# Kernel tuning notes

Measured on AMD Instinct MI355X. Metric: run time of the kernel, lower is better.

The kernel has to match this reference:

```python
import jax, jax.numpy as jnp
import numpy as np

B, T, D, H = 4, 2048, 1024, 16
DH = D // H  # head dim = 64

def setup_inputs() -> dict:
    key = jax.random.key(0)
    k1, k2, k3, k4, k5, k6 = jax.random.split(key, 6)
    x = jax.random.normal(k1, (B, T, D), dtype=jnp.float32)
    mask = jax.random.randint(k2, (B, 1, 1, T), 0, 2, dtype=jnp.int32)
    # nn.Linear(out_dim, out_dim*3): weight stored here as [in, out]
    W_qkv = jax.random.normal(k3, (D, 3 * D), dtype=jnp.float32) * (1.0 / np.sqrt(D))
    b_qkv = jax.random.normal(k4, (3 * D,), dtype=jnp.float32) * 0.02
    W_out = jax.random.normal(k5, (D, D), dtype=jnp.float32) * (1.0 / np.sqrt(D))
    b_out = jax.random.normal(k6, (D,), dtype=jnp.float32) * 0.02
    return {"x": x, "mask": mask, "W_qkv": W_qkv, "b_qkv": b_qkv,
            "W_out": W_out, "b_out": b_out}

def reference(x, mask, W_qkv, b_qkv, W_out, b_out):
    # QKV projection: [B,T,3D]
    qkv = x @ W_qkv + b_qkv
    q, k, v = qkv[..., :D], qkv[..., D:2 * D], qkv[..., 2 * D:]
    # split heads -> [B,H,T,DH]
    def split(t):
        return t.reshape(B, T, H, DH).transpose(0, 2, 1, 3)
    q, k, v = split(q), split(k), split(v)
    # scaled dot-product attention (scale = sqrt(head_dim), per torch source)
    scores = jnp.einsum('bhqd,bhkd->bhqk', q, k) / jnp.sqrt(jnp.float32(DH))
    scores = jnp.where(mask == 0, jnp.float32(-1000.0), scores)
    weights = jax.nn.softmax(scores, axis=-1)  # dropout = identity (eval mode)
    out = jnp.einsum('bhqk,bhkd->bhqd', weights, v)
    out = out.transpose(0, 2, 1, 3).reshape(B, T, D)
    return out @ W_out + b_out
```

## Files before the change

### kernel.cpp

```cpp
#include <hip/hip_runtime.h>
#include <hip/hip_bf16.h>
#include <stdint.h>

#define B_  4
#define T_  2048
#define D_  1024
#define H_  16
#define DH_ 64

typedef _Float16 half8 __attribute__((ext_vector_type(8)));
typedef _Float16 half4 __attribute__((ext_vector_type(4)));
typedef float    f32x4 __attribute__((ext_vector_type(4)));

#define MFMA16(a, b, c) __builtin_amdgcn_mfma_f32_16x16x32_f16(a, b, c, 0, 0, 0)

__device__ static inline void gload_lds16(const void* g, void* l) {
  __builtin_amdgcn_global_load_lds(
      (const __attribute__((address_space(1))) void*)g,
      (__attribute__((address_space(3))) void*)l, 16, 0, 0);
}

__global__ void convert_f32_f16(const float* __restrict__ in, _Float16* __restrict__ out, long n) {
  long i = ((long)blockIdx.x * blockDim.x + threadIdx.x) * 4;
  long stride = (long)gridDim.x * blockDim.x * 4;
  for (; i < n; i += stride) {
    float4 v = *(const float4*)(in + i);
    half4 hv;
    hv.x = (_Float16)v.x; hv.y = (_Float16)v.y; hv.z = (_Float16)v.z; hv.w = (_Float16)v.w;
    *(half4*)(out + i) = hv;
  }
}

__global__ void make_maskh(const int* __restrict__ mask, _Float16* __restrict__ mh, int n) {
  int i = blockIdx.x * blockDim.x + threadIdx.x;
  if (i < n) mh[i] = mask[i] ? (_Float16)1.0f : (_Float16)0.0f;
}

__global__ void transpose_f32_f16(const float* __restrict__ in, _Float16* __restrict__ out,
                                  int K, int N) {
  __shared__ float tile[32][33];
  int n0 = blockIdx.x * 32, k0 = blockIdx.y * 32;
  int x = threadIdx.x, y = threadIdx.y;
  #pragma unroll
  for (int j = 0; j < 32; j += 8)
    tile[y + j][x] = in[(long)(k0 + y + j) * N + n0 + x];
  __syncthreads();
  #pragma unroll
  for (int j = 0; j < 32; j += 8)
    out[(long)(n0 + y + j) * K + k0 + x] = (_Float16)tile[x][y + j];
}

__global__ void vtrans_kernel(const _Float16* __restrict__ V, const _Float16* __restrict__ mh,
                              _Float16* __restrict__ Vt) {
  __shared__ _Float16 tl[64 * 73];
  const int t0 = blockIdx.x * 64;
  const int bh = blockIdx.y, b = bh >> 4;
  const long base = (long)bh * (T_ * DH_);
  const int t = threadIdx.x;
  #pragma unroll
  for (int i = 0; i < 2; ++i) {
    int c = t + i * 256;
    int row = c >> 3, cg = c & 7;
    _Float16 m = mh[b * T_ + t0 + row];
    half8 vv = *(const half8*)(V + base + (long)(t0 + row) * DH_ + cg * 8);
    #pragma unroll
    for (int j = 0; j < 8; ++j) vv[j] = vv[j] * m;
    *(half8*)&tl[row * 73 + cg * 8] = vv;
  }
  __syncthreads();
  #pragma unroll
  for (int i = 0; i < 2; ++i) {
    int c = t + i * 256;
    int dr = c >> 3, tg = c & 7;
    half8 v;
    #pragma unroll
    for (int j = 0; j < 8; ++j) v[j] = tl[(tg * 8 + j) * 73 + dr];
    *(half8*)(Vt + base + (long)dr * T_ + t0 + tg * 8) = v;
  }
}

template <int EPI>
__global__ __launch_bounds__(256, 2)
void mha_gemm(const _Float16* __restrict__ A, const _Float16* __restrict__ Bt,
              const float* __restrict__ bias,
              _Float16* __restrict__ qo, _Float16* __restrict__ ko, _Float16* __restrict__ vo,
              float* __restrict__ co, int M, int N, int K) {
  __shared__ _Float16 As[128 * 32];
  __shared__ _Float16 Bs[128 * 32];
  const int t = threadIdx.x;
  const int l = t & 63;
  const int w = t >> 6;
  const int wr = w >> 1, wc = w & 1;
  const int m0 = blockIdx.y * 128, n0 = blockIdx.x * 128;

  const _Float16* ag0 = A  + (long)(m0 +      w * 16 + (l >> 2)) * K + (l & 3) * 8;
  const _Float16* ag1 = A  + (long)(m0 + 64 + w * 16 + (l >> 2)) * K + (l & 3) * 8;
  const _Float16* bg0 = Bt + (long)(n0 +      w * 16 + (l >> 2)) * K + (l & 3) * 8;
  const _Float16* bg1 = Bt + (long)(n0 + 64 + w * 16 + (l >> 2)) * K + (l & 3) * 8;
  _Float16* la0 = &As[w * 512];
  _Float16* la1 = &As[2048 + w * 512];
  _Float16* lb0 = &Bs[w * 512];
  _Float16* lb1 = &Bs[2048 + w * 512];

  f32x4 acc[4][4];
  #pragma unroll
  for (int f = 0; f < 4; ++f)
    #pragma unroll
    for (int g = 0; g < 4; ++g) acc[f][g] = (f32x4){0.f, 0.f, 0.f, 0.f};

  const int ar = (wr * 64 + (l & 15)) * 32 + (l >> 4) * 8;
  const int br = (wc * 64 + (l & 15)) * 32 + (l >> 4) * 8;

  for (int k0 = 0; k0 < K; k0 += 32) {
    gload_lds16(ag0 + k0, la0);
    gload_lds16(ag1 + k0, la1);
    gload_lds16(bg0 + k0, lb0);
    gload_lds16(bg1 + k0, lb1);
    __syncthreads();
    half8 af[4], bf[4];
    #pragma unroll
    for (int f = 0; f < 4; ++f) af[f] = *(const half8*)&As[ar + f * 16 * 32];
    #pragma unroll
    for (int g = 0; g < 4; ++g) bf[g] = *(const half8*)&Bs[br + g * 16 * 32];
    #pragma unroll
    for (int f = 0; f < 4; ++f)
      #pragma unroll
      for (int g = 0; g < 4; ++g)
        acc[f][g] = MFMA16(af[f], bf[g], acc[f][g]);
    __syncthreads();
  }

  if constexpr (EPI == 0) {
    #pragma unroll
    for (int g = 0; g < 4; ++g) {
      int j = n0 + wc * 64 + g * 16 + (l & 15);
      float bv = bias[j];
      int which = j >> 10;
      int d = j & 1023;
      int h = d >> 6, dh = d & 63;
      _Float16* base = which == 0 ? qo : (which == 1 ? ko : vo);
      float sc = which == 0 ? 0.1803368801f : 1.0f;
      #pragma unroll
      for (int f = 0; f < 4; ++f) {
        int row0 = m0 + wr * 64 + f * 16 + ((l >> 4) << 2);
        #pragma unroll
        for (int r = 0; r < 4; ++r) {
          int row = row0 + r;
          int bb = row >> 11, tt = row & 2047;
          base[(((long)bb * H_ + h) * T_ + tt) * DH_ + dh] =
              (_Float16)((acc[f][g][r] + bv) * sc);
        }
      }
    }
  } else {
    #pragma unroll
    for (int g = 0; g < 4; ++g) {
      int j = n0 + wc * 64 + g * 16 + (l & 15);
      float bv = bias[j];
      #pragma unroll
      for (int f = 0; f < 4; ++f) {
        int row0 = m0 + wr * 64 + f * 16 + ((l >> 4) << 2);
        #pragma unroll
        for (int r = 0; r < 4; ++r)
          co[(long)(row0 + r) * N + j] = acc[f][g][r] + bv;
      }
    }
  }
}

__global__ __launch_bounds__(128, 2)
void mha_attn3(const _Float16* __restrict__ Q, const _Float16* __restrict__ K,
               const _Float16* __restrict__ Vt, const _Float16* __restrict__ mh,
               _Float16* __restrict__ out) {
  __shared__ _Float16 Ksh[2][4096];
  const int t = threadIdx.x, l = t & 63, w = t >> 6;
  const int hi = l >> 4, q = l & 15;

  const int bid = blockIdx.x;
  const int idx = bid >> 3;
  const int bh = (bid & 7) * 8 + (idx >> 4);
  const int qt = idx & 15;
  const int b = bh >> 4, h = bh & 15;
  const long base = (long)bh * (T_ * DH_);
  const int qb = qt * 128 + w * 64;

  half8 qf[4][2];
  #pragma unroll
  for (int G = 0; G < 4; ++G) {
    qf[G][0] = *(const half8*)(Q + base + (long)(qb + G * 16 + q) * DH_ + hi * 8);
    qf[G][1] = *(const half8*)(Q + base + (long)(qb + G * 16 + q) * DH_ + hi * 8 + 32);
  }

  const _Float16* ks[4];
  #pragma unroll
  for (int j = 0; j < 4; ++j) {
    int c = w * 256 + j * 64 + l;
    int row = c >> 3, sub = c & 7;
    int s = (sub ^ ((row & 7) ^ ((row >> 2) & 7))) * 8;
    ks[j] = K + base + row * DH_ + s;
  }

  int kcb[4];
  #pragma unroll
  for (int g = 0; g < 4; ++g) {
    int kr = (g >> 1) * 32 + (q >> 2) * 8 + (g & 1) * 4 + (q & 3);
    int sw = (kr & 7) ^ ((kr >> 2) & 7);
    kcb[g] = kr * 128 + ((hi * 16) ^ (sw << 4));
  }

  const _Float16* vsrc[4];
  #pragma unroll
  for (int o = 0; o < 4; ++o)
    vsrc[o] = Vt + base + (long)(o * 16 + q) * T_ + hi * 8;
  const _Float16* mrow = mh + b * T_ + hi * 8;

  f32x4 acc[4][4], accD[4];
  #pragma unroll
  for (int G = 0; G < 4; ++G) {
    accD[G] = (f32x4){0.f, 0.f, 0.f, 0.f};
    #pragma unroll
    for (int o = 0; o < 4; ++o) acc[G][o] = (f32x4){0.f, 0.f, 0.f, 0.f};
  }

  #pragma unroll
  for (int j = 0; j < 4; ++j)
    gload_lds16(ks[j], &Ksh[0][w * 2048 + j * 512]);
  __syncthreads();

  for (int kt = 0; kt < T_ / 64; ++kt) {
    const int bi = kt & 1;
    if (kt + 1 < T_ / 64) {
      #pragma unroll
      for (int j = 0; j < 4; ++j)
        gload_lds16(ks[j] + (kt + 1) * (64 * DH_), &Ksh[bi ^ 1][w * 2048 + j * 512]);
    }

    half8 vf[4][2];
    #pragma unroll
    for (int o = 0; o < 4; ++o) {
      vf[o][0] = *(const half8*)(vsrc[o] + kt * 64);
      vf[o][1] = *(const half8*)(vsrc[o] + kt * 64 + 32);
    }
    const half8 mf0 = *(const half8*)(mrow + kt * 64);
    const half8 mf1 = *(const half8*)(mrow + kt * 64 + 32);

    const char* kbb = (const char*)Ksh[bi];
    half8 kf[4][2];
    #pragma unroll
    for (int g = 0; g < 4; ++g) {
      kf[g][0] = *(const half8*)(kbb + kcb[g]);
      kf[g][1] = *(const half8*)(kbb + (kcb[g] ^ 64));
    }

    #pragma unroll
    for (int G = 0; G < 4; ++G) {
      f32x4 z[4];
      #pragma unroll
      for (int g = 0; g < 4; ++g) {
        f32x4 zz = (f32x4){0.f, 0.f, 0.f, 0.f};
        zz = MFMA16(kf[g][0], qf[G][0], zz);
        z[g] = MFMA16(kf[g][1], qf[G][1], zz);
      }
      half8 p0, p1;
      #pragma unroll
      for (int r = 0; r < 4; ++r) {
        p0[r]     = (_Float16)__builtin_amdgcn_exp2f(z[0][r]);
        p0[4 + r] = (_Float16)__builtin_amdgcn_exp2f(z[1][r]);
        p1[r]     = (_Float16)__builtin_amdgcn_exp2f(z[2][r]);
        p1[4 + r] = (_Float16)__builtin_amdgcn_exp2f(z[3][r]);
      }
      accD[G] = MFMA16(p0, mf0, accD[G]);
      accD[G] = MFMA16(p1, mf1, accD[G]);
      #pragma unroll
      for (int o = 0; o < 4; ++o) {
        acc[G][o] = MFMA16(p0, vf[o][0], acc[G][o]);
        acc[G][o] = MFMA16(p1, vf[o][1], acc[G][o]);
      }
    }
    __syncthreads();
  }

  #pragma unroll
  for (int G = 0; G < 4; ++G)
    #pragma unroll
    for (int r = 0; r < 4; ++r) {
      float inv = __builtin_amdgcn_rcpf(accD[G][r]);
      int trow = qb + G * 16 + hi * 4 + r;
      #pragma unroll
      for (int o = 0; o < 4; ++o)
        out[((long)b * T_ + trow) * D_ + h * DH_ + o * 16 + q] =
            (_Float16)(acc[G][o][r] * inv);
    }
}

extern "C" void kernel_launch(void* const* d_in, const int* in_sizes, int n_in,
                              void* d_out, int out_size, void* d_ws, size_t ws_size,
                              hipStream_t stream) {
  const float* x    = (const float*)d_in[0];
  const int*   mask = (const int*)d_in[1];
  const float* wqkv = (const float*)d_in[2];
  const float* bqkv = (const float*)d_in[3];
  const float* wout = (const float*)d_in[4];
  const float* bout = (const float*)d_in[5];
  float* out = (float*)d_out;

  _Float16* ws = (_Float16*)d_ws;
  const long nX = (long)B_ * T_ * D_;
  _Float16* xh    = ws;
  _Float16* wqkvt = xh + nX;
  _Float16* woutt = wqkvt + (long)D_ * 3 * D_;
  _Float16* mh    = woutt + (long)D_ * D_;
  _Float16* Qb    = woutt + (long)D_ * D_ + 16384;
  _Float16* Kb    = Qb + nX;
  _Float16* Vb    = Kb + nX;
  _Float16* attnh = Vb + nX;
  _Float16* Vtg   = xh;

  convert_f32_f16<<<2048, 256, 0, stream>>>(x, xh, nX);
  make_maskh<<<(B_ * T_) / 256, 256, 0, stream>>>(mask, mh, B_ * T_);
  transpose_f32_f16<<<dim3(3 * D_ / 32, D_ / 32), dim3(32, 8), 0, stream>>>(wqkv, wqkvt, D_, 3 * D_);
  transpose_f32_f16<<<dim3(D_ / 32, D_ / 32), dim3(32, 8), 0, stream>>>(wout, woutt, D_, D_);

  mha_gemm<0><<<dim3(3 * D_ / 128, B_ * T_ / 128), 256, 0, stream>>>(
      xh, wqkvt, bqkv, Qb, Kb, Vb, nullptr, B_ * T_, 3 * D_, D_);

  vtrans_kernel<<<dim3(T_ / 64, B_ * H_), 256, 0, stream>>>(Vb, mh, Vtg);

  mha_attn3<<<1024, 128, 0, stream>>>(Qb, Kb, Vtg, mh, attnh);

  mha_gemm<1><<<dim3(D_ / 128, B_ * T_ / 128), 256, 0, stream>>>(
      attnh, woutt, bout, nullptr, nullptr, nullptr, out, B_ * T_, D_, D_);
}
```

Before: 208.5 us.

## Deepen GEMM K-tile with swizzled LDS, remap blocks, halve attention query tile

The GEMM now loads 64-wide K tiles into XOR-swizzled LDS, which halves the number of barriers per K and avoids bank conflicts. It also maps a 1D grid so that consecutive blocks spread across XCDs, aiming for better L2 locality. The attention kernel processes 32 query rows per wave instead of 64, doubling the grid to 2048 blocks and lowering register pressure. It also raises wave priority around the MFMA section and packs the exp results with cvt_pkrtz. The cost is that each K/V tile is loaded twice as many times overall in attention, and the LDS footprint of the GEMM doubles.

```diff
diff --git a/kernel.cpp b/kernel.cpp
--- a/kernel.cpp
+++ b/kernel.cpp
@@ -10,6 +10,7 @@
 
 typedef _Float16 half8 __attribute__((ext_vector_type(8)));
 typedef _Float16 half4 __attribute__((ext_vector_type(4)));
+typedef __fp16   fp16x2 __attribute__((ext_vector_type(2)));
 typedef float    f32x4 __attribute__((ext_vector_type(4)));
 
 #define MFMA16(a, b, c) __builtin_amdgcn_mfma_f32_16x16x32_f16(a, b, c, 0, 0, 0)
@@ -81,26 +82,31 @@
 
 template <int EPI>
 __global__ __launch_bounds__(256, 2)
-void mha_gemm(const _Float16* __restrict__ A, const _Float16* __restrict__ Bt,
-              const float* __restrict__ bias,
-              _Float16* __restrict__ qo, _Float16* __restrict__ ko, _Float16* __restrict__ vo,
-              float* __restrict__ co, int M, int N, int K) {
-  __shared__ _Float16 As[128 * 32];
-  __shared__ _Float16 Bs[128 * 32];
+void mha_gemm2(const _Float16* __restrict__ A, const _Float16* __restrict__ Bt,
+               const float* __restrict__ bias,
+               _Float16* __restrict__ qo, _Float16* __restrict__ ko, _Float16* __restrict__ vo,
+               float* __restrict__ co, int M, int N, int K, int gx) {
+  __shared__ _Float16 As[128 * 64];
+  __shared__ _Float16 Bs[128 * 64];
   const int t = threadIdx.x;
   const int l = t & 63;
   const int w = t >> 6;
   const int wr = w >> 1, wc = w & 1;
-  const int m0 = blockIdx.y * 128, n0 = blockIdx.x * 128;
-
-  const _Float16* ag0 = A  + (long)(m0 +      w * 16 + (l >> 2)) * K + (l & 3) * 8;
-  const _Float16* ag1 = A  + (long)(m0 + 64 + w * 16 + (l >> 2)) * K + (l & 3) * 8;
-  const _Float16* bg0 = Bt + (long)(n0 +      w * 16 + (l >> 2)) * K + (l & 3) * 8;
-  const _Float16* bg1 = Bt + (long)(n0 + 64 + w * 16 + (l >> 2)) * K + (l & 3) * 8;
-  _Float16* la0 = &As[w * 512];
-  _Float16* la1 = &As[2048 + w * 512];
-  _Float16* lb0 = &Bs[w * 512];
-  _Float16* lb1 = &Bs[2048 + w * 512];
+
+  const int cpx = gridDim.x >> 3;
+  const int wg = (blockIdx.x & 7) * cpx + (blockIdx.x >> 3);
+  const int m0 = (wg / gx) * 128, n0 = (wg % gx) * 128;
+
+  const _Float16* ag[4];
+  const _Float16* bg[4];
+  #pragma unroll
+  for (int j = 0; j < 4; ++j) {
+    int c = j * 256 + t;
+    int row = c >> 3, sub = c & 7;
+    int s = (sub ^ (row & 7)) * 8;
+    ag[j] = A  + (long)(m0 + row) * K + s;
+    bg[j] = Bt + (long)(n0 + row) * K + s;
+  }
 
   f32x4 acc[4][4];
   #pragma unroll
@@ -108,25 +114,34 @@
     #pragma unroll
     for (int g = 0; g < 4; ++g) acc[f][g] = (f32x4){0.f, 0.f, 0.f, 0.f};
 
-  const int ar = (wr * 64 + (l & 15)) * 32 + (l >> 4) * 8;
-  const int br = (wc * 64 + (l & 15)) * 32 + (l >> 4) * 8;
-
-  for (int k0 = 0; k0 < K; k0 += 32) {
-    gload_lds16(ag0 + k0, la0);
-    gload_lds16(ag1 + k0, la1);
-    gload_lds16(bg0 + k0, lb0);
-    gload_lds16(bg1 + k0, lb1);
+  const int hi = l >> 4;
+
+  for (int k0 = 0; k0 < K; k0 += 64) {
+    #pragma unroll
+    for (int j = 0; j < 4; ++j) {
+      gload_lds16(ag[j] + k0, &As[j * 2048 + w * 512]);
+      gload_lds16(bg[j] + k0, &Bs[j * 2048 + w * 512]);
+    }
     __syncthreads();
-    half8 af[4], bf[4];
-    #pragma unroll
-    for (int f = 0; f < 4; ++f) af[f] = *(const half8*)&As[ar + f * 16 * 32];
-    #pragma unroll
-    for (int g = 0; g < 4; ++g) bf[g] = *(const half8*)&Bs[br + g * 16 * 32];
-    #pragma unroll
-    for (int f = 0; f < 4; ++f)
-      #pragma unroll
-      for (int g = 0; g < 4; ++g)
-        acc[f][g] = MFMA16(af[f], bf[g], acc[f][g]);
+    half8 af[2][4], bf[2][4];
+    #pragma unroll
+    for (int kk = 0; kk < 2; ++kk)
+      #pragma unroll
+      for (int f = 0; f < 4; ++f) {
+        int ra = wr * 64 + f * 16 + (l & 15);
+        int rb = wc * 64 + f * 16 + (l & 15);
+        af[kk][f] = *(const half8*)((const char*)As + ra * 128 +
+                                    ((((kk << 2) | hi) ^ (ra & 7)) << 4));
+        bf[kk][f] = *(const half8*)((const char*)Bs + rb * 128 +
+                                    ((((kk << 2) | hi) ^ (rb & 7)) << 4));
+      }
+    #pragma unroll
+    for (int kk = 0; kk < 2; ++kk)
+      #pragma unroll
+      for (int f = 0; f < 4; ++f)
+        #pragma unroll
+        for (int g = 0; g < 4; ++g)
+          acc[f][g] = MFMA16(af[kk][f], bf[kk][g], acc[f][g]);
     __syncthreads();
   }
 
@@ -169,7 +184,7 @@
 }
 
 __global__ __launch_bounds__(128, 2)
-void mha_attn3(const _Float16* __restrict__ Q, const _Float16* __restrict__ K,
+void mha_attn4(const _Float16* __restrict__ Q, const _Float16* __restrict__ K,
                const _Float16* __restrict__ Vt, const _Float16* __restrict__ mh,
                _Float16* __restrict__ out) {
   __shared__ _Float16 Ksh[2][4096];
@@ -178,15 +193,15 @@
 
   const int bid = blockIdx.x;
   const int idx = bid >> 3;
-  const int bh = (bid & 7) * 8 + (idx >> 4);
-  const int qt = idx & 15;
+  const int bh = (bid & 7) * 8 + (idx >> 5);
+  const int qt = idx & 31;
   const int b = bh >> 4, h = bh & 15;
   const long base = (long)bh * (T_ * DH_);
-  const int qb = qt * 128 + w * 64;
-
-  half8 qf[4][2];
-  #pragma unroll
-  for (int G = 0; G < 4; ++G) {
+  const int qb = qt * 64 + w * 32;
+
+  half8 qf[2][2];
+  #pragma unroll
+  for (int G = 0; G < 2; ++G) {
     qf[G][0] = *(const half8*)(Q + base + (long)(qb + G * 16 + q) * DH_ + hi * 8);
     qf[G][1] = *(const half8*)(Q + base + (long)(qb + G * 16 + q) * DH_ + hi * 8 + 32);
   }
@@ -214,9 +229,9 @@
     vsrc[o] = Vt + base + (long)(o * 16 + q) * T_ + hi * 8;
   const _Float16* mrow = mh + b * T_ + hi * 8;
 
-  f32x4 acc[4][4], accD[4];
-  #pragma unroll
-  for (int G = 0; G < 4; ++G) {
+  f32x4 acc[2][4], accD[2];
+  #pragma unroll
+  for (int G = 0; G < 2; ++G) {
     accD[G] = (f32x4){0.f, 0.f, 0.f, 0.f};
     #pragma unroll
     for (int o = 0; o < 4; ++o) acc[G][o] = (f32x4){0.f, 0.f, 0.f, 0.f};
@@ -252,8 +267,9 @@
       kf[g][1] = *(const half8*)(kbb + (kcb[g] ^ 64));
     }
 
-    #pragma unroll
-    for (int G = 0; G < 4; ++G) {
+    __builtin_amdgcn_s_setprio(1);
+    #pragma unroll
+    for (int G = 0; G < 2; ++G) {
       f32x4 z[4];
       #pragma unroll
       for (int g = 0; g < 4; ++g) {
@@ -261,27 +277,32 @@
         zz = MFMA16(kf[g][0], qf[G][0], zz);
         z[g] = MFMA16(kf[g][1], qf[G][1], zz);
       }
-      half8 p0, p1;
-      #pragma unroll
-      for (int r = 0; r < 4; ++r) {
-        p0[r]     = (_Float16)__builtin_amdgcn_exp2f(z[0][r]);
-        p0[4 + r] = (_Float16)__builtin_amdgcn_exp2f(z[1][r]);
-        p1[r]     = (_Float16)__builtin_amdgcn_exp2f(z[2][r]);
-        p1[4 + r] = (_Float16)__builtin_amdgcn_exp2f(z[3][r]);
-      }
-      accD[G] = MFMA16(p0, mf0, accD[G]);
-      accD[G] = MFMA16(p1, mf1, accD[G]);
+      union { fp16x2 h2[4]; half8 h8; } u0, u1;
+      #pragma unroll
+      for (int i = 0; i < 2; ++i) {
+        u0.h2[i]     = __builtin_amdgcn_cvt_pkrtz(__builtin_amdgcn_exp2f(z[0][2*i]),
+                                                  __builtin_amdgcn_exp2f(z[0][2*i+1]));
+        u0.h2[2 + i] = __builtin_amdgcn_cvt_pkrtz(__builtin_amdgcn_exp2f(z[1][2*i]),
+                                                  __builtin_amdgcn_exp2f(z[1][2*i+1]));
+        u1.h2[i]     = __builtin_amdgcn_cvt_pkrtz(__builtin_amdgcn_exp2f(z[2][2*i]),
+                                                  __builtin_amdgcn_exp2f(z[2][2*i+1]));
+        u1.h2[2 + i] = __builtin_amdgcn_cvt_pkrtz(__builtin_amdgcn_exp2f(z[3][2*i]),
+                                                  __builtin_amdgcn_exp2f(z[3][2*i+1]));
+      }
+      accD[G] = MFMA16(u0.h8, mf0, accD[G]);
+      accD[G] = MFMA16(u1.h8, mf1, accD[G]);
       #pragma unroll
       for (int o = 0; o < 4; ++o) {
-        acc[G][o] = MFMA16(p0, vf[o][0], acc[G][o]);
-        acc[G][o] = MFMA16(p1, vf[o][1], acc[G][o]);
-      }
-    }
+        acc[G][o] = MFMA16(u0.h8, vf[o][0], acc[G][o]);
+        acc[G][o] = MFMA16(u1.h8, vf[o][1], acc[G][o]);
+      }
+    }
+    __builtin_amdgcn_s_setprio(0);
     __syncthreads();
   }
 
   #pragma unroll
-  for (int G = 0; G < 4; ++G)
+  for (int G = 0; G < 2; ++G)
     #pragma unroll
     for (int r = 0; r < 4; ++r) {
       float inv = __builtin_amdgcn_rcpf(accD[G][r]);
@@ -321,13 +342,13 @@
   transpose_f32_f16<<<dim3(3 * D_ / 32, D_ / 32), dim3(32, 8), 0, stream>>>(wqkv, wqkvt, D_, 3 * D_);
   transpose_f32_f16<<<dim3(D_ / 32, D_ / 32), dim3(32, 8), 0, stream>>>(wout, woutt, D_, D_);
 
-  mha_gemm<0><<<dim3(3 * D_ / 128, B_ * T_ / 128), 256, 0, stream>>>(
-      xh, wqkvt, bqkv, Qb, Kb, Vb, nullptr, B_ * T_, 3 * D_, D_);
+  mha_gemm2<0><<<1536, 256, 0, stream>>>(
+      xh, wqkvt, bqkv, Qb, Kb, Vb, nullptr, B_ * T_, 3 * D_, D_, 24);
 
   vtrans_kernel<<<dim3(T_ / 64, B_ * H_), 256, 0, stream>>>(Vb, mh, Vtg);
 
-  mha_attn3<<<1024, 128, 0, stream>>>(Qb, Kb, Vtg, mh, attnh);
-
-  mha_gemm<1><<<dim3(D_ / 128, B_ * T_ / 128), 256, 0, stream>>>(
-      attnh, woutt, bout, nullptr, nullptr, nullptr, out, B_ * T_, D_, D_);
-}
+  mha_attn4<<<2048, 128, 0, stream>>>(Qb, Kb, Vtg, mh, attnh);
+
+  mha_gemm2<1><<<512, 256, 0, stream>>>(
+      attnh, woutt, bout, nullptr, nullptr, nullptr, out, B_ * T_, D_, D_, 8);
+}
```

Result: slower. 275.1 us (+31.9%).
